# Optimization experiments

Hardware: AMD Instinct MI355X
Metric: run time of the kernel (lower is better)

## Reference

```python
import jax, jax.numpy as jnp
import numpy as np

B, H, W, D, K = 64, 32, 32, 128, 1024


def setup_inputs() -> dict:
    key = jax.random.key(0)
    k1, k2 = jax.random.split(key)
    z_e = jax.random.normal(k1, (B, H, W, D), dtype=jnp.float32)
    # GlorotUniform over (k, d): limit = sqrt(6 / (k + d))
    limit = float(np.sqrt(6.0 / (K + D)))
    codebook = jax.random.uniform(k2, (K, D), dtype=jnp.float32, minval=-limit, maxval=limit)
    return {"z_e": z_e, "codebook": codebook}


def reference(z_e, codebook):
    # Original: norm = ||z_e[..., None, :] - codebook||_2 over d, then argmin over k.
    # Squared distance has the same argmin; expand to avoid the (B,H,W,k,d) tensor:
    # ||z - c||^2 = ||z||^2 - 2 z.c + ||c||^2
    z2 = jnp.sum(z_e * z_e, axis=-1, keepdims=True)           # (B,H,W,1)
    c2 = jnp.sum(codebook * codebook, axis=-1)                # (k,)
    dots = jnp.einsum('bhwd,kd->bhwk', z_e, codebook)         # (B,H,W,k)
    dist2 = z2 - 2.0 * dots + c2                              # (B,H,W,k)
    q_z = jnp.argmin(dist2, axis=-1)                          # (B,H,W) int
    return q_z
```

## Files before the change

### kernel.cpp

```cpp
#include <hip/hip_runtime.h>
#include <stdint.h>

#define NPTS   65536
#define DDIM   128
#define KCODES 1024

typedef __attribute__((ext_vector_type(8))) _Float16  half8;
typedef __attribute__((ext_vector_type(4))) float     f32x4;
typedef __attribute__((ext_vector_type(2))) _Float16  half2v;

__device__ __forceinline__ void split16(float x, _Float16& hi, _Float16& lo) {
  _Float16 h = (__builtin_fabsf(x) < 6.103515625e-05f) ? (_Float16)0.f : (_Float16)x;
  hi = h;
  lo = (_Float16)(__fmul_rn(__fsub_rn(x, (float)h), 2048.f));
}

__device__ __forceinline__ float np_sumsq_128(const float* __restrict__ row) {
  float r[8];
#pragma unroll
  for (int k = 0; k < 8; ++k) r[k] = __fmul_rn(row[k], row[k]);
  for (int i = 8; i < 128; i += 8)
#pragma unroll
    for (int k = 0; k < 8; ++k) r[k] = __fadd_rn(r[k], __fmul_rn(row[i + k], row[i + k]));
  float s01 = __fadd_rn(r[0], r[1]), s23 = __fadd_rn(r[2], r[3]);
  float s45 = __fadd_rn(r[4], r[5]), s67 = __fadd_rn(r[6], r[7]);
  return __fadd_rn(__fadd_rn(s01, s23), __fadd_rn(s45, s67));
}

__device__ __forceinline__ void async_copy16(const void* g, void* l) {
  auto gp = (const __attribute__((address_space(1))) unsigned int*)(uintptr_t)g;
  auto lp = (__attribute__((address_space(3))) unsigned int*)(unsigned)(uintptr_t)l;
  __builtin_amdgcn_global_load_lds(gp, lp, 16, 0, 0);
}

constexpr size_t SZ_B   = (size_t)KCODES * DDIM * 2;
constexpr size_t OFF_B1 = 0;
constexpr size_t OFF_B2 = SZ_B;
constexpr size_t OFF_Z2 = 2 * SZ_B;
constexpr size_t OFF_C2 = OFF_Z2 + (size_t)NPTS * 4;
constexpr size_t WS_NEED = OFF_C2 + (size_t)KCODES * 4;

__global__ __launch_bounds__(256) void vq_prep_cb(const float* __restrict__ cb,
                                                  _Float16* __restrict__ B1,
                                                  _Float16* __restrict__ B2,
                                                  float* __restrict__ c2) {
  const int w = threadIdx.x >> 6, ln = threadIdx.x & 63;
  const int code = blockIdx.x * 4 + w;
  const float2 cv = ((const float2*)(cb + (size_t)code * DDIM))[ln];
  _Float16 h0, l0, h1, l1;
  split16(cv.x, h0, l0); split16(cv.y, h1, l1);
  const int kg = ln >> 2;
  const int o  = 2 * (ln & 3);
  const size_t dst = (size_t)code * DDIM + (size_t)((kg ^ (code & 15)) * 8 + o);
  *(half2v*)(B1 + dst) = (half2v){h0, h1};
  *(half2v*)(B2 + dst) = (half2v){l0, l1};

  if (threadIdx.x < 32) {
    const int cc = blockIdx.x * 4 + (threadIdx.x >> 3), jj = threadIdx.x & 7;
    const float* row = cb + (size_t)cc * DDIM;
    float e = row[jj];
    float acc = __fmul_rn(e, e);
    for (int i = 1; i < 16; ++i) {
      e = row[i * 8 + jj];
      acc = __fadd_rn(acc, __fmul_rn(e, e));
    }
    float a1 = __fadd_rn(acc, __shfl_xor(acc, 1));
    float a2 = __fadd_rn(a1, __shfl_xor(a1, 2));
    float a4 = __fadd_rn(a2, __shfl_xor(a2, 4));
    if (jj == 0) c2[cc] = a4;
  }
}

__global__ __launch_bounds__(256) void vq_z2(const float4* __restrict__ z4,
                                             float* __restrict__ z2) {
  __shared__ float Ls[32 * 132];
  const int tid = threadIdx.x;
  const size_t base4 = (size_t)blockIdx.x * 1024;
#pragma unroll
  for (int j = 0; j < 4; ++j) {
    const int idx = tid + j * 256;
    float4 v = z4[base4 + idx];
    *(float4*)&Ls[(idx >> 5) * 132 + (idx & 31) * 4] = v;
  }
  __syncthreads();
  const int r = tid >> 3, jj = tid & 7;
  const float* row = &Ls[r * 132];
  float e = row[jj];
  float acc = __fmul_rn(e, e);
  for (int i = 1; i < 16; ++i) {
    e = row[i * 8 + jj];
    acc = __fadd_rn(acc, __fmul_rn(e, e));
  }
  float a1 = __fadd_rn(acc, __shfl_xor(acc, 1));
  float a2 = __fadd_rn(a1, __shfl_xor(a1, 2));
  float a4 = __fadd_rn(a2, __shfl_xor(a2, 4));
  if (jj == 0) z2[blockIdx.x * 32 + r] = a4;
}

__global__ __launch_bounds__(256, 2) void vq_gemm(
    const float* __restrict__ z,
    const unsigned short* __restrict__ B1g, const unsigned short* __restrict__ B2g,
    const float* __restrict__ z2, const float* __restrict__ c2,
    int* __restrict__ out) {
  __shared__ alignas(16) unsigned short Bs1[64 * 128];
  __shared__ alignas(16) unsigned short Bs2[64 * 128];
  const int tid = threadIdx.x;
  const int ln = tid & 63, w = tid >> 6;
  const int wr = w >> 1, wc = w & 1;
  const int l15 = ln & 15, q = ln >> 4;
  const size_t row0 = (size_t)blockIdx.x * 128;

  half8 a1f[4][4], a2f[4][4];
#pragma unroll
  for (int rf = 0; rf < 4; ++rf) {
    const float* zr = z + (row0 + wr * 64 + rf * 16 + l15) * DDIM;
#pragma unroll
    for (int ks = 0; ks < 4; ++ks) {
      float tmp[8];
      *(float4*)tmp       = *(const float4*)(zr + ks * 32 + q * 8);
      *(float4*)(tmp + 4) = *(const float4*)(zr + ks * 32 + q * 8 + 4);
      half8 h, l;
#pragma unroll
      for (int e = 0; e < 8; ++e) {
        _Float16 hh, ll;
        split16(tmp[e], hh, ll);
        h[e] = hh; l[e] = ll;
      }
      a1f[rf][ks] = h; a2f[rf][ks] = l;
    }
  }

#pragma unroll
  for (int j = 0; j < 4; ++j) {
    const int s = tid + j * 256;
    async_copy16(B2g + s * 8, Bs2 + s * 8);
    async_copy16(B1g + s * 8, Bs1 + s * 8);
  }

  float mv[16];
  int mi[16];
#pragma unroll
  for (int i = 0; i < 16; ++i) { mv[i] = 3.0e38f; mi[i] = 0; }

  __syncthreads();

  for (int iter = 0; iter < 16; ++iter) {
    const int c0 = iter * 64;
    f32x4 acc[4][2];
#pragma unroll
    for (int rf = 0; rf < 4; ++rf)
#pragma unroll
      for (int cf = 0; cf < 2; ++cf) acc[rf][cf] = (f32x4){0.f, 0.f, 0.f, 0.f};

#pragma unroll
    for (int ks = 0; ks < 4; ++ks) {
      half8 b[2];
#pragma unroll
      for (int cf = 0; cf < 2; ++cf)
        b[cf] = *(const half8*)&Bs2[(wc * 32 + cf * 16 + l15) * 128 +
                                    (((ks * 4 + q) ^ l15) * 8)];
#pragma unroll
      for (int rf = 0; rf < 4; ++rf)
#pragma unroll
        for (int cf = 0; cf < 2; ++cf)
          acc[rf][cf] = __builtin_amdgcn_mfma_f32_16x16x32_f16(a1f[rf][ks], b[cf],
                                                               acc[rf][cf], 0, 0, 0);
    }

    __syncthreads();
    if (iter < 15) {
#pragma unroll
      for (int j = 0; j < 4; ++j) {
        const int s = tid + j * 256;
        async_copy16(B2g + (size_t)(c0 + 64) * DDIM + s * 8, Bs2 + s * 8);
      }
    }

#pragma unroll
    for (int ks = 0; ks < 4; ++ks) {
      half8 b[2];
#pragma unroll
      for (int cf = 0; cf < 2; ++cf)
        b[cf] = *(const half8*)&Bs1[(wc * 32 + cf * 16 + l15) * 128 +
                                    (((ks * 4 + q) ^ l15) * 8)];
#pragma unroll
      for (int rf = 0; rf < 4; ++rf)
#pragma unroll
        for (int cf = 0; cf < 2; ++cf)
          acc[rf][cf] = __builtin_amdgcn_mfma_f32_16x16x32_f16(a2f[rf][ks], b[cf],
                                                               acc[rf][cf], 0, 0, 0);
    }
#pragma unroll
    for (int rf = 0; rf < 4; ++rf)
#pragma unroll
      for (int cf = 0; cf < 2; ++cf) acc[rf][cf] = acc[rf][cf] * 4.8828125e-4f;

#pragma unroll
    for (int ks = 0; ks < 4; ++ks) {
      half8 b[2];
#pragma unroll
      for (int cf = 0; cf < 2; ++cf)
        b[cf] = *(const half8*)&Bs1[(wc * 32 + cf * 16 + l15) * 128 +
                                    (((ks * 4 + q) ^ l15) * 8)];
#pragma unroll
      for (int rf = 0; rf < 4; ++rf)
#pragma unroll
        for (int cf = 0; cf < 2; ++cf)
          acc[rf][cf] = __builtin_amdgcn_mfma_f32_16x16x32_f16(a1f[rf][ks], b[cf],
                                                               acc[rf][cf], 0, 0, 0);
    }

#pragma unroll
    for (int rf = 0; rf < 4; ++rf)
#pragma unroll
      for (int reg = 0; reg < 4; ++reg) {
        const int slot = rf * 4 + reg;
        const float z2v = z2[row0 + wr * 64 + rf * 16 + q * 4 + reg];
#pragma unroll
        for (int cf = 0; cf < 2; ++cf) {
          const float c2v = c2[c0 + wc * 32 + cf * 16 + l15];
          float dot = acc[rf][cf][reg];
          float v = __fadd_rn(__fsub_rn(z2v, __fmul_rn(2.f, dot)), c2v);
          int idx = c0 + wc * 32 + cf * 16 + l15;
          if (v < mv[slot]) { mv[slot] = v; mi[slot] = idx; }
        }
      }

    __syncthreads();
    if (iter < 15) {
#pragma unroll
      for (int j = 0; j < 4; ++j) {
        const int s = tid + j * 256;
        async_copy16(B1g + (size_t)(c0 + 64) * DDIM + s * 8, Bs1 + s * 8);
      }
    }
  }

#pragma unroll
  for (int slot = 0; slot < 16; ++slot) {
    float v = mv[slot];
    int i = mi[slot];
#pragma unroll
    for (int m = 1; m <= 8; m <<= 1) {
      float ov = __shfl_xor(v, m);
      int oi = __shfl_xor(i, m);
      if (ov < v || (ov == v && oi < i)) { v = ov; i = oi; }
    }
    mv[slot] = v; mi[slot] = i;
  }

  float* rv = (float*)Bs1;
  int* ri = (int*)(Bs1 + 4096);
  if (l15 == 0) {
#pragma unroll
    for (int rf = 0; rf < 4; ++rf)
#pragma unroll
      for (int reg = 0; reg < 4; ++reg) {
        const int row = wr * 64 + rf * 16 + q * 4 + reg;
        rv[row * 2 + wc] = mv[rf * 4 + reg];
        ri[row * 2 + wc] = mi[rf * 4 + reg];
      }
  }
  __syncthreads();
  if (tid < 128) {
    float v0 = rv[tid * 2 + 0], v1 = rv[tid * 2 + 1];
    int i0 = ri[tid * 2 + 0], i1 = ri[tid * 2 + 1];
    int i = (v1 < v0 || (v1 == v0 && i1 < i0)) ? i1 : i0;
    out[row0 + tid] = i;
  }
}

__global__ __launch_bounds__(256) void vq_fallback(const float* __restrict__ z,
                                                   const float* __restrict__ cb,
                                                   int* __restrict__ out) {
  __shared__ float zs[DDIM];
  __shared__ float z2s;
  __shared__ float bv[256];
  __shared__ int bi[256];
  const int p = blockIdx.x, tid = threadIdx.x;
  if (tid < DDIM) zs[tid] = z[(size_t)p * DDIM + tid];
  __syncthreads();
  if (tid == 0) z2s = np_sumsq_128(zs);
  __syncthreads();
  const float z2p = z2s;
  float best = 3.0e38f;
  int bidx = 0;
  for (int c = tid; c < KCODES; c += 256) {
    const float* cr = cb + (size_t)c * DDIM;
    double acc = 0.0;
#pragma unroll 8
    for (int d = 0; d < DDIM; ++d) acc += (double)zs[d] * (double)cr[d];
    float dfl = (float)acc;
    float c2k = np_sumsq_128(cr);
    float v = __fadd_rn(__fsub_rn(z2p, __fmul_rn(2.f, dfl)), c2k);
    if (v < best) { best = v; bidx = c; }
  }
  bv[tid] = best; bi[tid] = bidx;
  __syncthreads();
  for (int off = 128; off > 0; off >>= 1) {
    if (tid < off) {
      if (bv[tid + off] < bv[tid] || (bv[tid + off] == bv[tid] && bi[tid + off] < bi[tid])) {
        bv[tid] = bv[tid + off]; bi[tid] = bi[tid + off];
      }
    }
    __syncthreads();
  }
  if (tid == 0) out[p] = bi[0];
}

extern "C" void kernel_launch(void* const* d_in, const int* in_sizes, int n_in,
                              void* d_out, int out_size, void* d_ws, size_t ws_size,
                              hipStream_t stream) {
  (void)in_sizes; (void)n_in; (void)out_size;
  const float* z = (const float*)d_in[0];
  const float* cb = (const float*)d_in[1];
  int* out = (int*)d_out;

  if (d_ws != nullptr && ws_size >= WS_NEED) {
    char* ws = (char*)d_ws;
    _Float16* B1 = (_Float16*)(ws + OFF_B1);
    _Float16* B2 = (_Float16*)(ws + OFF_B2);
    float* z2 = (float*)(ws + OFF_Z2);
    float* c2 = (float*)(ws + OFF_C2);

    vq_prep_cb<<<KCODES / 4, 256, 0, stream>>>(cb, B1, B2, c2);
    vq_z2<<<NPTS / 32, 256, 0, stream>>>((const float4*)z, z2);
    vq_gemm<<<NPTS / 128, 256, 0, stream>>>(
        z, (const unsigned short*)(ws + OFF_B1), (const unsigned short*)(ws + OFF_B2),
        z2, c2, out);
  } else {
    vq_fallback<<<NPTS, 256, 0, stream>>>(z, cb, out);
  }
}
```

Measured before the change: 137.9 us.

## Fuse z-norm computation into GEMM kernel and re-tile warps to full codebook columns

```diff
diff --git a/kernel.cpp b/kernel.cpp
--- a/kernel.cpp
+++ b/kernel.cpp
@@ -7,6 +7,7 @@
 
 typedef __attribute__((ext_vector_type(8))) _Float16  half8;
 typedef __attribute__((ext_vector_type(4))) float     f32x4;
+typedef __attribute__((ext_vector_type(4))) int       int4v;
 typedef __attribute__((ext_vector_type(2))) _Float16  half2v;
 
 __device__ __forceinline__ void split16(float x, _Float16& hi, _Float16& lo) {
@@ -36,8 +37,7 @@
 constexpr size_t SZ_B   = (size_t)KCODES * DDIM * 2;
 constexpr size_t OFF_B1 = 0;
 constexpr size_t OFF_B2 = SZ_B;
-constexpr size_t OFF_Z2 = 2 * SZ_B;
-constexpr size_t OFF_C2 = OFF_Z2 + (size_t)NPTS * 4;
+constexpr size_t OFF_C2 = 2 * SZ_B;
 constexpr size_t WS_NEED = OFF_C2 + (size_t)KCODES * 4;
 
 __global__ __launch_bounds__(256) void vq_prep_cb(const float* __restrict__ cb,
@@ -71,49 +71,60 @@
   }
 }
 
-__global__ __launch_bounds__(256) void vq_z2(const float4* __restrict__ z4,
-                                             float* __restrict__ z2) {
-  __shared__ float Ls[32 * 132];
-  const int tid = threadIdx.x;
-  const size_t base4 = (size_t)blockIdx.x * 1024;
-#pragma unroll
-  for (int j = 0; j < 4; ++j) {
-    const int idx = tid + j * 256;
-    float4 v = z4[base4 + idx];
-    *(float4*)&Ls[(idx >> 5) * 132 + (idx & 31) * 4] = v;
-  }
-  __syncthreads();
-  const int r = tid >> 3, jj = tid & 7;
-  const float* row = &Ls[r * 132];
-  float e = row[jj];
-  float acc = __fmul_rn(e, e);
-  for (int i = 1; i < 16; ++i) {
-    e = row[i * 8 + jj];
-    acc = __fadd_rn(acc, __fmul_rn(e, e));
-  }
-  float a1 = __fadd_rn(acc, __shfl_xor(acc, 1));
-  float a2 = __fadd_rn(a1, __shfl_xor(a1, 2));
-  float a4 = __fadd_rn(a2, __shfl_xor(a2, 4));
-  if (jj == 0) z2[blockIdx.x * 32 + r] = a4;
-}
-
 __global__ __launch_bounds__(256, 2) void vq_gemm(
     const float* __restrict__ z,
     const unsigned short* __restrict__ B1g, const unsigned short* __restrict__ B2g,
-    const float* __restrict__ z2, const float* __restrict__ c2,
-    int* __restrict__ out) {
-  __shared__ alignas(16) unsigned short Bs1[64 * 128];
-  __shared__ alignas(16) unsigned short Bs2[64 * 128];
+    const float* __restrict__ c2g, int* __restrict__ out) {
+  __shared__ alignas(16) char smem[16384 + 16384 + 4096 + 512];
+  unsigned short* Bs1 = (unsigned short*)smem;
+  unsigned short* Bs2 = (unsigned short*)(smem + 16384);
+  float* c2sh = (float*)(smem + 32768);
+  float* z2sh = (float*)(smem + 32768 + 4096);
+  float* Ls   = (float*)smem;
+
   const int tid = threadIdx.x;
-  const int ln = tid & 63, w = tid >> 6;
-  const int wr = w >> 1, wc = w & 1;
+  const int ln = tid & 63, wr = tid >> 6;
   const int l15 = ln & 15, q = ln >> 4;
   const size_t row0 = (size_t)blockIdx.x * 128;
-
-  half8 a1f[4][4], a2f[4][4];
-#pragma unroll
-  for (int rf = 0; rf < 4; ++rf) {
-    const float* zr = z + (row0 + wr * 64 + rf * 16 + l15) * DDIM;
+  const float4* z4 = (const float4*)z;
+
+  for (int cc = 0; cc < 4; ++cc) {
+#pragma unroll
+    for (int j = 0; j < 4; ++j) {
+      const int idx = tid + j * 256;
+      float4 v = z4[(row0 + cc * 32) * 32 + idx];
+      *(float4*)&Ls[(idx >> 5) * 132 + (idx & 31) * 4] = v;
+    }
+    __syncthreads();
+    {
+      const int r = tid >> 3, jj = tid & 7;
+      const float* row = &Ls[r * 132];
+      float e = row[jj];
+      float acc = __fmul_rn(e, e);
+      for (int i = 1; i < 16; ++i) {
+        e = row[i * 8 + jj];
+        acc = __fadd_rn(acc, __fmul_rn(e, e));
+      }
+      float a1 = __fadd_rn(acc, __shfl_xor(acc, 1));
+      float a2 = __fadd_rn(a1, __shfl_xor(a1, 2));
+      float a4 = __fadd_rn(a2, __shfl_xor(a2, 4));
+      if (jj == 0) z2sh[cc * 32 + r] = a4;
+    }
+    __syncthreads();
+  }
+
+#pragma unroll
+  for (int j = 0; j < 4; ++j) {
+    const int s = tid + j * 256;
+    async_copy16(B2g + s * 8, Bs2 + s * 8);
+    async_copy16(B1g + s * 8, Bs1 + s * 8);
+  }
+  async_copy16(c2g + tid * 4, c2sh + tid * 4);
+
+  half8 a1f[2][4], a2f[2][4];
+#pragma unroll
+  for (int rf = 0; rf < 2; ++rf) {
+    const float* zr = z + (row0 + wr * 32 + rf * 16 + l15) * DDIM;
 #pragma unroll
     for (int ks = 0; ks < 4; ++ks) {
       float tmp[8];
@@ -130,39 +141,38 @@
     }
   }
 
-#pragma unroll
-  for (int j = 0; j < 4; ++j) {
-    const int s = tid + j * 256;
-    async_copy16(B2g + s * 8, Bs2 + s * 8);
-    async_copy16(B1g + s * 8, Bs1 + s * 8);
-  }
-
-  float mv[16];
-  int mi[16];
-#pragma unroll
-  for (int i = 0; i < 16; ++i) { mv[i] = 3.0e38f; mi[i] = 0; }
+  float mv[8];
+  int mi[8];
+#pragma unroll
+  for (int i = 0; i < 8; ++i) { mv[i] = 3.0e38f; mi[i] = 0; }
 
   __syncthreads();
+
+  float z2r[8];
+#pragma unroll
+  for (int rf = 0; rf < 2; ++rf)
+#pragma unroll
+    for (int reg = 0; reg < 4; ++reg)
+      z2r[rf * 4 + reg] = z2sh[wr * 32 + rf * 16 + q * 4 + reg];
 
   for (int iter = 0; iter < 16; ++iter) {
     const int c0 = iter * 64;
-    f32x4 acc[4][2];
-#pragma unroll
-    for (int rf = 0; rf < 4; ++rf)
-#pragma unroll
-      for (int cf = 0; cf < 2; ++cf) acc[rf][cf] = (f32x4){0.f, 0.f, 0.f, 0.f};
+    f32x4 acc[2][4];
+#pragma unroll
+    for (int rf = 0; rf < 2; ++rf)
+#pragma unroll
+      for (int cf = 0; cf < 4; ++cf) acc[rf][cf] = (f32x4){0.f, 0.f, 0.f, 0.f};
 
 #pragma unroll
     for (int ks = 0; ks < 4; ++ks) {
-      half8 b[2];
-#pragma unroll
-      for (int cf = 0; cf < 2; ++cf)
-        b[cf] = *(const half8*)&Bs2[(wc * 32 + cf * 16 + l15) * 128 +
-                                    (((ks * 4 + q) ^ l15) * 8)];
-#pragma unroll
-      for (int rf = 0; rf < 4; ++rf)
-#pragma unroll
-        for (int cf = 0; cf < 2; ++cf)
+      half8 b[4];
+#pragma unroll
+      for (int cf = 0; cf < 4; ++cf)
+        b[cf] = *(const half8*)&Bs2[(cf * 16 + l15) * 128 + (((ks * 4 + q) ^ l15) * 8)];
+#pragma unroll
+      for (int rf = 0; rf < 2; ++rf)
+#pragma unroll
+        for (int cf = 0; cf < 4; ++cf)
           acc[rf][cf] = __builtin_amdgcn_mfma_f32_16x16x32_f16(a1f[rf][ks], b[cf],
                                                                acc[rf][cf], 0, 0, 0);
     }
@@ -178,50 +188,48 @@
 
 #pragma unroll
     for (int ks = 0; ks < 4; ++ks) {
-      half8 b[2];
-#pragma unroll
-      for (int cf = 0; cf < 2; ++cf)
-        b[cf] = *(const half8*)&Bs1[(wc * 32 + cf * 16 + l15) * 128 +
-                                    (((ks * 4 + q) ^ l15) * 8)];
-#pragma unroll
-      for (int rf = 0; rf < 4; ++rf)
-#pragma unroll
-        for (int cf = 0; cf < 2; ++cf)
+      half8 b[4];
+#pragma unroll
+      for (int cf = 0; cf < 4; ++cf)
+        b[cf] = *(const half8*)&Bs1[(cf * 16 + l15) * 128 + (((ks * 4 + q) ^ l15) * 8)];
+#pragma unroll
+      for (int rf = 0; rf < 2; ++rf)
+#pragma unroll
+        for (int cf = 0; cf < 4; ++cf)
           acc[rf][cf] = __builtin_amdgcn_mfma_f32_16x16x32_f16(a2f[rf][ks], b[cf],
                                                                acc[rf][cf], 0, 0, 0);
     }
 #pragma unroll
-    for (int rf = 0; rf < 4; ++rf)
-#pragma unroll
-      for (int cf = 0; cf < 2; ++cf) acc[rf][cf] = acc[rf][cf] * 4.8828125e-4f;
+    for (int rf = 0; rf < 2; ++rf)
+#pragma unroll
+      for (int cf = 0; cf < 4; ++cf) acc[rf][cf] = acc[rf][cf] * 4.8828125e-4f;
 
 #pragma unroll
     for (int ks = 0; ks < 4; ++ks) {
-      half8 b[2];
-#pragma unroll
-      for (int cf = 0; cf < 2; ++cf)
-        b[cf] = *(const half8*)&Bs1[(wc * 32 + cf * 16 + l15) * 128 +
-                                    (((ks * 4 + q) ^ l15) * 8)];
-#pragma unroll
-      for (int rf = 0; rf < 4; ++rf)
-#pragma unroll
-        for (int cf = 0; cf < 2; ++cf)
+      half8 b[4];
+#pragma unroll
+      for (int cf = 0; cf < 4; ++cf)
+        b[cf] = *(const half8*)&Bs1[(cf * 16 + l15) * 128 + (((ks * 4 + q) ^ l15) * 8)];
+#pragma unroll
+      for (int rf = 0; rf < 2; ++rf)
+#pragma unroll
+        for (int cf = 0; cf < 4; ++cf)
           acc[rf][cf] = __builtin_amdgcn_mfma_f32_16x16x32_f16(a1f[rf][ks], b[cf],
                                                                acc[rf][cf], 0, 0, 0);
     }
 
 #pragma unroll
-    for (int rf = 0; rf < 4; ++rf)
+    for (int rf = 0; rf < 2; ++rf)
 #pragma unroll
       for (int reg = 0; reg < 4; ++reg) {
         const int slot = rf * 4 + reg;
-        const float z2v = z2[row0 + wr * 64 + rf * 16 + q * 4 + reg];
-#pragma unroll
-        for (int cf = 0; cf < 2; ++cf) {
-          const float c2v = c2[c0 + wc * 32 + cf * 16 + l15];
+        const float z2v = z2r[slot];
+#pragma unroll
+        for (int cf = 0; cf < 4; ++cf) {
+          const float c2v = c2sh[c0 + cf * 16 + l15];
           float dot = acc[rf][cf][reg];
           float v = __fadd_rn(__fsub_rn(z2v, __fmul_rn(2.f, dot)), c2v);
-          int idx = c0 + wc * 32 + cf * 16 + l15;
+          int idx = c0 + cf * 16 + l15;
           if (v < mv[slot]) { mv[slot] = v; mi[slot] = idx; }
         }
       }
@@ -237,7 +245,7 @@
   }
 
 #pragma unroll
-  for (int slot = 0; slot < 16; ++slot) {
+  for (int slot = 0; slot < 8; ++slot) {
     float v = mv[slot];
     int i = mi[slot];
 #pragma unroll
@@ -249,24 +257,12 @@
     mv[slot] = v; mi[slot] = i;
   }
 
-  float* rv = (float*)Bs1;
-  int* ri = (int*)(Bs1 + 4096);
   if (l15 == 0) {
 #pragma unroll
-    for (int rf = 0; rf < 4; ++rf)
-#pragma unroll
-      for (int reg = 0; reg < 4; ++reg) {
-        const int row = wr * 64 + rf * 16 + q * 4 + reg;
-        rv[row * 2 + wc] = mv[rf * 4 + reg];
-        ri[row * 2 + wc] = mi[rf * 4 + reg];
-      }
-  }
-  __syncthreads();
-  if (tid < 128) {
-    float v0 = rv[tid * 2 + 0], v1 = rv[tid * 2 + 1];
-    int i0 = ri[tid * 2 + 0], i1 = ri[tid * 2 + 1];
-    int i = (v1 < v0 || (v1 == v0 && i1 < i0)) ? i1 : i0;
-    out[row0 + tid] = i;
+    for (int rf = 0; rf < 2; ++rf) {
+      int4v r = {mi[rf * 4 + 0], mi[rf * 4 + 1], mi[rf * 4 + 2], mi[rf * 4 + 3]};
+      *(int4v*)&out[row0 + wr * 32 + rf * 16 + q * 4] = r;
+    }
   }
 }
 
@@ -320,14 +316,12 @@
     char* ws = (char*)d_ws;
     _Float16* B1 = (_Float16*)(ws + OFF_B1);
     _Float16* B2 = (_Float16*)(ws + OFF_B2);
-    float* z2 = (float*)(ws + OFF_Z2);
     float* c2 = (float*)(ws + OFF_C2);
 
     vq_prep_cb<<<KCODES / 4, 256, 0, stream>>>(cb, B1, B2, c2);
-    vq_z2<<<NPTS / 32, 256, 0, stream>>>((const float4*)z, z2);
     vq_gemm<<<NPTS / 128, 256, 0, stream>>>(
         z, (const unsigned short*)(ws + OFF_B1), (const unsigned short*)(ws + OFF_B2),
-        z2, c2, out);
+        c2, out);
   } else {
     vq_fallback<<<NPTS, 256, 0, stream>>>(z, cb, out);
   }
```

Result: faster. 118.5 us (-14.0%).
